# Kernel optimization log

Measured on AMD Instinct MI355X. Metric: run time of the kernel, lower is better.

Reference implementation:

```python
import jax, jax.numpy as jnp
import numpy as np

B, M, T, L, K = 64, 16, 2048, 64, 32
N = T - L + 1  # 1985 sliding-window positions


def setup_inputs() -> dict:
    key = jax.random.key(0)
    k1, k2, k3 = jax.random.split(key, 3)
    x = jax.random.normal(k1, (B, M, T), dtype=jnp.float32)
    # shapelets initialized uniform(-1, 1) as in nn.init.uniform_
    shapelets = jax.random.uniform(k2, (K, L), dtype=jnp.float32, minval=-1.0, maxval=1.0)
    # penalty maps (learned; zeros at init, random here for a non-trivial weighting)
    penalty_maps = 0.1 * jax.random.normal(k3, (K, M, N), dtype=jnp.float32)
    return {"x": x, "shapelets": shapelets, "penalty_maps": penalty_maps}


def reference(x, shapelets, penalty_maps):
    # x: (B, M, T); shapelets: (K, L); penalty_maps: (K, M, N)
    Lw = shapelets.shape[1]
    n_pos = x.shape[2] - Lw + 1
    # sliding-window view: (B, M, N, L), equivalent to torch unfold(dim=2, size=L, step=1)
    idx = jnp.arange(n_pos)[:, None] + jnp.arange(Lw)[None, :]
    sub = x[:, :, idx]  # (B, M, N, L)

    def per_shapelet(args):
        shp, pmap = args  # (L,), (M, N)
        # raw squared L2 distance over window, per channel/position: (B, M, N)
        raw = jnp.sum((sub - shp[None, None, None, :]) ** 2, axis=3)
        pen = jax.nn.elu(-pmap) + 2.0  # (M, N)
        wd = jnp.sum(raw * pen[None], axis=1)  # sum over channels -> (B, N)
        return jnp.min(wd, axis=1)  # min over positions -> (B,)

    # sequential map over the K shapelets avoids a Kx blow-up of the (B,M,N,L) intermediate
    feats = jax.lax.map(per_shapelet, (shapelets, penalty_maps))  # (K, B)
    return feats.T  # (B, K)
```

## Files before the change

### kernel.cpp

```cpp
#include <hip/hip_runtime.h>
#include <hip/hip_bf16.h>

#define B_ 64
#define M_ 16
#define T_ 2048
#define L_ 64
#define K_ 32
#define N_ (T_ - L_ + 1)
#define KMN (K_ * M_ * N_)
#define TN 64
#define NTH 256
#define XROW 144
#define STSTR 72
#define SQSTR 64

typedef __attribute__((ext_vector_type(8))) short bf16x8;
typedef __attribute__((ext_vector_type(4))) float f32x4;

__device__ __forceinline__ unsigned short f2bf(float f) {
    __hip_bfloat16 h = __float2bfloat16(f);
    return __builtin_bit_cast(unsigned short, h);
}

__global__ void pen_init_kernel(const float* __restrict__ pmap,
                                const float* __restrict__ shp,
                                float* __restrict__ pen,
                                float* __restrict__ ss_ws,
                                unsigned* __restrict__ out) {
    const int gid = blockIdx.x * 256 + threadIdx.x;
    if (gid < B_ * K_) out[gid] = 0x7F800000u;
    if (gid < K_) {
        float s = 0.f;
        for (int l = 0; l < L_; ++l) { float v = shp[gid * L_ + l]; s = fmaf(v, v, s); }
        ss_ws[gid] = s;
    }
    if (gid < KMN / 4) {
        const int i4 = gid * 4;
        float4 p = *(const float4*)(pmap + i4);
        float4 r;
        r.x = (p.x < 0.f) ? (2.f - p.x) : (__expf(-p.x) + 1.f);
        r.y = (p.y < 0.f) ? (2.f - p.y) : (__expf(-p.y) + 1.f);
        r.z = (p.z < 0.f) ? (2.f - p.z) : (__expf(-p.z) + 1.f);
        r.w = (p.w < 0.f) ? (2.f - p.w) : (__expf(-p.w) + 1.f);
        *(float4*)(pen + i4) = r;
    }
}

__global__ __launch_bounds__(NTH, 2)
void shapelet_mfma_kernel(const float* __restrict__ x,
                          const float* __restrict__ shp,
                          const float* __restrict__ pen,
                          const float* __restrict__ ss_ws,
                          unsigned* __restrict__ out) {
    __shared__ __align__(16) unsigned short xbuf4[M_][4][XROW];
    __shared__ __align__(16) unsigned short st[K_][STSTR];
    __shared__ __align__(16) float sqw[M_][SQSTR];

    const int tid = threadIdx.x;
    const int n0 = blockIdx.x * TN;
    const int b  = blockIdx.y;
    const bool fast = (n0 + 128 <= T_);

    const float* xb = x + ((size_t)b * M_) * T_ + n0;
    for (int g = tid; g < M_ * 31; g += NTH) {
        const int m = g / 31, j4 = (g - m * 31) * 4;
        const float* src = xb + m * T_ + j4;
        float h[8];
        if (fast) {
            float4 v0 = *(const float4*)src;
            float4 v1 = *(const float4*)(src + 4);
            h[0] = v0.x; h[1] = v0.y; h[2] = v0.z; h[3] = v0.w;
            h[4] = v1.x; h[5] = v1.y; h[6] = v1.z; h[7] = v1.w;
        } else {
#pragma unroll
            for (int i = 0; i < 8; ++i)
                h[i] = (n0 + j4 + i < T_) ? src[i] : 0.f;
        }
        unsigned short hb[8];
#pragma unroll
        for (int i = 0; i < 8; ++i) hb[i] = f2bf(h[i]);
#pragma unroll
        for (int s = 0; s < 4; ++s) {
            ushort4 sv = { hb[s], hb[s + 1], hb[s + 2], hb[s + 3] };
            *(ushort4*)&xbuf4[m][s][j4] = sv;
        }
    }
    for (int i = tid; i < K_ * 16; i += NTH) {
        const int k = i >> 4, l4 = (i & 15) * 4;
        float4 v = *(const float4*)(shp + k * L_ + l4);
        ushort4 sv = { f2bf(v.x), f2bf(v.y), f2bf(v.z), f2bf(v.w) };
        *(ushort4*)&st[k][l4] = sv;
    }
    if (tid < M_ * 8) {
        const int m = tid >> 3, j0 = (tid & 7) * 8;
        const float* xr = x + ((size_t)b * M_ + m) * T_ + n0;
        float s = 0.f;
        if (fast) {
#pragma unroll
            for (int qd = 0; qd < 16; ++qd) {
                float4 v = *(const float4*)(xr + j0 + qd * 4);
                s = fmaf(v.x, v.x, s); s = fmaf(v.y, v.y, s);
                s = fmaf(v.z, v.z, s); s = fmaf(v.w, v.w, s);
            }
            sqw[m][j0] = s;
#pragma unroll
            for (int d = 1; d < 8; ++d) {
                float a = xr[j0 + d + L_ - 1], r = xr[j0 + d - 1];
                s += a * a - r * r;
                sqw[m][j0 + d] = s;
            }
        } else {
            for (int l = 0; l < L_; ++l) {
                float v = (n0 + j0 + l < T_) ? xr[j0 + l] : 0.f;
                s = fmaf(v, v, s);
            }
            sqw[m][j0] = s;
            for (int d = 1; d < 8; ++d) {
                float a = (n0 + j0 + d + L_ - 1 < T_) ? xr[j0 + d + L_ - 1] : 0.f;
                float r = (n0 + j0 + d - 1 < T_) ? xr[j0 + d - 1] : 0.f;
                s += a * a - r * r;
                sqw[m][j0 + d] = s;
            }
        }
    }
    __syncthreads();

    const int lane = tid & 63;
    const int w  = tid >> 6;
    const int rl = lane & 15;
    const int q  = lane >> 4;
    const int sp = rl & 3;
    const int e0 = 16 * w + 8 * q + (rl & ~3);
    const int eq = e0 >> 2;
    const int nrow = n0 + 16 * w + 4 * q;

    bf16x8 bfr[2][2];
#pragma unroll
    for (int t = 0; t < 2; ++t)
#pragma unroll
        for (int h = 0; h < 2; ++h)
            bfr[t][h] = *(const bf16x8*)&st[16 * t + rl][8 * q + 32 * h];

    const float ssk0 = ss_ws[rl], ssk1 = ss_ws[16 + rl];

    const float* pr0 = pen + (size_t)rl * (M_ * N_) + nrow;
    const float* pr1 = pr0 + (size_t)16 * M_ * N_;

    f32x4 wd0 = (f32x4)0.f, wd1 = (f32x4)0.f;
    const f32x4 zero = (f32x4)0.f;

#pragma unroll 2
    for (int m = 0; m < M_; ++m) {
        float4 p0, p1;
        if (fast) {
            p0 = *(const float4*)(pr0 + (size_t)m * N_);
            p1 = *(const float4*)(pr1 + (size_t)m * N_);
        } else {
            p0 = make_float4(2.f, 2.f, 2.f, 2.f);
            p1 = make_float4(2.f, 2.f, 2.f, 2.f);
            const float* r0_ = pr0 + (size_t)m * N_;
            const float* r1_ = pr1 + (size_t)m * N_;
            if (nrow     < N_) { p0.x = r0_[0]; p1.x = r1_[0]; }
            if (nrow + 1 < N_) { p0.y = r0_[1]; p1.y = r1_[1]; }
            if (nrow + 2 < N_) { p0.z = r0_[2]; p1.z = r1_[2]; }
            if (nrow + 3 < N_) { p0.w = r0_[3]; p1.w = r1_[3]; }
        }

        const uint2* prow = (const uint2*)&xbuf4[m][sp][0];
        uint2 lo0 = prow[eq],     hi0 = prow[eq + 1];
        uint2 lo1 = prow[eq + 8], hi1 = prow[eq + 9];
        union { uint2 u2[2]; bf16x8 v; } fa0, fa1;
        fa0.u2[0] = lo0; fa0.u2[1] = hi0;
        fa1.u2[0] = lo1; fa1.u2[1] = hi1;

        f32x4 c0_ = __builtin_amdgcn_mfma_f32_16x16x32_bf16(fa0.v, bfr[0][0], zero, 0, 0, 0);
        c0_       = __builtin_amdgcn_mfma_f32_16x16x32_bf16(fa1.v, bfr[0][1], c0_, 0, 0, 0);
        f32x4 c1_ = __builtin_amdgcn_mfma_f32_16x16x32_bf16(fa0.v, bfr[1][0], zero, 0, 0, 0);
        c1_       = __builtin_amdgcn_mfma_f32_16x16x32_bf16(fa1.v, bfr[1][1], c1_, 0, 0, 0);

        f32x4 sq = *(const f32x4*)&sqw[m][16 * w + 4 * q];
        const float pe0[4] = { p0.x, p0.y, p0.z, p0.w };
        const float pe1[4] = { p1.x, p1.y, p1.z, p1.w };
#pragma unroll
        for (int r = 0; r < 4; ++r) {
            float t0v = fmaf(-2.f, c0_[r], sq[r] + ssk0);
            wd0[r] = fmaf(pe0[r], t0v, wd0[r]);
            float t1v = fmaf(-2.f, c1_[r], sq[r] + ssk1);
            wd1[r] = fmaf(pe1[r], t1v, wd1[r]);
        }
    }

#pragma unroll
    for (int t = 0; t < 2; ++t) {
        float lmin = __int_as_float(0x7F800000);
        const f32x4& wdv = t ? wd1 : wd0;
#pragma unroll
        for (int r = 0; r < 4; ++r) {
            if (nrow + r < N_) lmin = fminf(lmin, wdv[r]);
        }
        lmin = fminf(lmin, __shfl_xor(lmin, 16));
        lmin = fminf(lmin, __shfl_xor(lmin, 32));
        if (q == 0) {
            atomicMin(out + (size_t)b * K_ + 16 * t + rl,
                      __float_as_uint(fmaxf(lmin, 0.f)));
        }
    }
}

extern "C" void kernel_launch(void* const* d_in, const int* in_sizes, int n_in,
                              void* d_out, int out_size, void* d_ws, size_t ws_size,
                              hipStream_t stream) {
    const float* x    = (const float*)d_in[0];
    const float* shp  = (const float*)d_in[1];
    const float* pmap = (const float*)d_in[2];
    unsigned* out = (unsigned*)d_out;
    float* pen   = (float*)d_ws;
    float* ss_ws = pen + KMN;

    pen_init_kernel<<<dim3((KMN / 4 + 255) / 256), dim3(256), 0, stream>>>(
        pmap, shp, pen, ss_ws, out);

    dim3 grid((N_ + TN - 1) / TN, B_);
    shapelet_mfma_kernel<<<grid, dim3(NTH), 0, stream>>>(x, shp, pen, ss_ws, out);
}
```

Baseline: 100.8 us.

## Fuse penalty transform into main kernel and process four batches per block

Each block now handles four batch items, so every penalty-map value loaded and transformed through ELU is reused across four batches instead of being re-read once per batch. The separate pen_init kernel is gone: the ELU transform is computed inline, the shapelet norms are computed in shared memory, and output initialisation becomes a memset. The shapelet-norm term is hoisted out of the channel loop as ssk times the summed penalty. Channels are staged in two halves to keep shared memory small, and a block-level min reduction replaces per-wave atomics. The trade-offs are a 4x smaller grid (512 blocks, which may underfill the GPU), extra barriers between the two channel halves, and redundant exp work across blocks.

Measured after the change: 110.4 us. +9.5%, slower.

```diff
diff --git a/kernel.cpp b/kernel.cpp
--- a/kernel.cpp
+++ b/kernel.cpp
@@ -7,12 +7,12 @@
 #define L_ 64
 #define K_ 32
 #define N_ (T_ - L_ + 1)
-#define KMN (K_ * M_ * N_)
 #define TN 64
 #define NTH 256
+#define NB 4
+#define MSPLIT 8
 #define XROW 144
 #define STSTR 72
-#define SQSTR 64
 
 typedef __attribute__((ext_vector_type(8))) short bf16x8;
 typedef __attribute__((ext_vector_type(4))) float f32x4;
@@ -22,78 +22,64 @@
     return __builtin_bit_cast(unsigned short, h);
 }
 
-__global__ void pen_init_kernel(const float* __restrict__ pmap,
-                                const float* __restrict__ shp,
-                                float* __restrict__ pen,
-                                float* __restrict__ ss_ws,
-                                unsigned* __restrict__ out) {
-    const int gid = blockIdx.x * 256 + threadIdx.x;
-    if (gid < B_ * K_) out[gid] = 0x7F800000u;
-    if (gid < K_) {
-        float s = 0.f;
-        for (int l = 0; l < L_; ++l) { float v = shp[gid * L_ + l]; s = fmaf(v, v, s); }
-        ss_ws[gid] = s;
-    }
-    if (gid < KMN / 4) {
-        const int i4 = gid * 4;
-        float4 p = *(const float4*)(pmap + i4);
-        float4 r;
-        r.x = (p.x < 0.f) ? (2.f - p.x) : (__expf(-p.x) + 1.f);
-        r.y = (p.y < 0.f) ? (2.f - p.y) : (__expf(-p.y) + 1.f);
-        r.z = (p.z < 0.f) ? (2.f - p.z) : (__expf(-p.z) + 1.f);
-        r.w = (p.w < 0.f) ? (2.f - p.w) : (__expf(-p.w) + 1.f);
-        *(float4*)(pen + i4) = r;
-    }
-}
-
 __global__ __launch_bounds__(NTH, 2)
 void shapelet_mfma_kernel(const float* __restrict__ x,
                           const float* __restrict__ shp,
-                          const float* __restrict__ pen,
-                          const float* __restrict__ ss_ws,
+                          const float* __restrict__ pmap,
                           unsigned* __restrict__ out) {
-    __shared__ __align__(16) unsigned short xbuf4[M_][4][XROW];
+    __shared__ __align__(16) unsigned short xbuf4[NB][MSPLIT][4][XROW];
     __shared__ __align__(16) unsigned short st[K_][STSTR];
-    __shared__ __align__(16) float sqw[M_][SQSTR];
+    __shared__ __align__(16) float sqw[NB][MSPLIT][TN];
+    __shared__ float ssb[K_];
 
     const int tid = threadIdx.x;
     const int n0 = blockIdx.x * TN;
-    const int b  = blockIdx.y;
-    const bool fast = (n0 + 128 <= T_);
-
-    const float* xb = x + ((size_t)b * M_) * T_ + n0;
-    for (int g = tid; g < M_ * 31; g += NTH) {
-        const int m = g / 31, j4 = (g - m * 31) * 4;
-        const float* src = xb + m * T_ + j4;
-        float h[8];
-        if (fast) {
-            float4 v0 = *(const float4*)src;
-            float4 v1 = *(const float4*)(src + 4);
-            h[0] = v0.x; h[1] = v0.y; h[2] = v0.z; h[3] = v0.w;
-            h[4] = v1.x; h[5] = v1.y; h[6] = v1.z; h[7] = v1.w;
-        } else {
-#pragma unroll
-            for (int i = 0; i < 8; ++i)
-                h[i] = (n0 + j4 + i < T_) ? src[i] : 0.f;
-        }
-        unsigned short hb[8];
-#pragma unroll
-        for (int i = 0; i < 8; ++i) hb[i] = f2bf(h[i]);
-#pragma unroll
-        for (int s = 0; s < 4; ++s) {
-            ushort4 sv = { hb[s], hb[s + 1], hb[s + 2], hb[s + 3] };
-            *(ushort4*)&xbuf4[m][s][j4] = sv;
-        }
-    }
+    const int b0 = blockIdx.y * NB;
+    const bool fast = (n0 + 2 * TN <= T_);
+
     for (int i = tid; i < K_ * 16; i += NTH) {
         const int k = i >> 4, l4 = (i & 15) * 4;
         float4 v = *(const float4*)(shp + k * L_ + l4);
         ushort4 sv = { f2bf(v.x), f2bf(v.y), f2bf(v.z), f2bf(v.w) };
         *(ushort4*)&st[k][l4] = sv;
     }
-    if (tid < M_ * 8) {
-        const int m = tid >> 3, j0 = (tid & 7) * 8;
-        const float* xr = x + ((size_t)b * M_ + m) * T_ + n0;
+    if (tid < K_) {
+        float s = 0.f;
+        for (int l = 0; l < L_; ++l) { float v = shp[tid * L_ + l]; s = fmaf(v, v, s); }
+        ssb[tid] = s;
+    }
+
+    auto stage = [&](int p) {
+        for (int g = tid; g < NB * MSPLIT * 31; g += NTH) {
+            const int bb = g / (MSPLIT * 31);
+            const int rem = g - bb * (MSPLIT * 31);
+            const int mm = rem / 31;
+            const int j4 = (rem - mm * 31) * 4;
+            const int m = p * MSPLIT + mm;
+            const float* src = x + ((size_t)(b0 + bb) * M_ + m) * T_ + n0 + j4;
+            float h[8];
+            if (fast) {
+                float4 v0 = *(const float4*)src;
+                float4 v1 = *(const float4*)(src + 4);
+                h[0] = v0.x; h[1] = v0.y; h[2] = v0.z; h[3] = v0.w;
+                h[4] = v1.x; h[5] = v1.y; h[6] = v1.z; h[7] = v1.w;
+            } else {
+#pragma unroll
+                for (int i = 0; i < 8; ++i)
+                    h[i] = (n0 + j4 + i < T_) ? src[i] : 0.f;
+            }
+            unsigned short hb[8];
+#pragma unroll
+            for (int i = 0; i < 8; ++i) hb[i] = f2bf(h[i]);
+#pragma unroll
+            for (int s = 0; s < 4; ++s) {
+                ushort4 sv = { hb[s], hb[s + 1], hb[s + 2], hb[s + 3] };
+                *(ushort4*)&xbuf4[bb][mm][s][j4] = sv;
+            }
+        }
+        const int bb = tid >> 6, mm = (tid >> 3) & 7, j0 = (tid & 7) * 8;
+        const int m = p * MSPLIT + mm;
+        const float* xr = x + ((size_t)(b0 + bb) * M_ + m) * T_ + n0;
         float s = 0.f;
         if (fast) {
 #pragma unroll
@@ -102,27 +88,29 @@
                 s = fmaf(v.x, v.x, s); s = fmaf(v.y, v.y, s);
                 s = fmaf(v.z, v.z, s); s = fmaf(v.w, v.w, s);
             }
-            sqw[m][j0] = s;
+            sqw[bb][mm][j0] = s;
 #pragma unroll
             for (int d = 1; d < 8; ++d) {
                 float a = xr[j0 + d + L_ - 1], r = xr[j0 + d - 1];
                 s += a * a - r * r;
-                sqw[m][j0 + d] = s;
+                sqw[bb][mm][j0 + d] = s;
             }
         } else {
             for (int l = 0; l < L_; ++l) {
                 float v = (n0 + j0 + l < T_) ? xr[j0 + l] : 0.f;
                 s = fmaf(v, v, s);
             }
-            sqw[m][j0] = s;
+            sqw[bb][mm][j0] = s;
             for (int d = 1; d < 8; ++d) {
                 float a = (n0 + j0 + d + L_ - 1 < T_) ? xr[j0 + d + L_ - 1] : 0.f;
                 float r = (n0 + j0 + d - 1 < T_) ? xr[j0 + d - 1] : 0.f;
                 s += a * a - r * r;
-                sqw[m][j0 + d] = s;
-            }
-        }
-    }
+                sqw[bb][mm][j0 + d] = s;
+            }
+        }
+    };
+
+    stage(0);
     __syncthreads();
 
     const int lane = tid & 63;
@@ -141,69 +129,108 @@
         for (int h = 0; h < 2; ++h)
             bfr[t][h] = *(const bf16x8*)&st[16 * t + rl][8 * q + 32 * h];
 
-    const float ssk0 = ss_ws[rl], ssk1 = ss_ws[16 + rl];
-
-    const float* pr0 = pen + (size_t)rl * (M_ * N_) + nrow;
+    const float ssk0 = ssb[rl], ssk1 = ssb[16 + rl];
+
+    const float* pr0 = pmap + (size_t)rl * (M_ * N_) + nrow;
     const float* pr1 = pr0 + (size_t)16 * M_ * N_;
 
-    f32x4 wd0 = (f32x4)0.f, wd1 = (f32x4)0.f;
+    f32x4 wd0[NB], wd1[NB];
+#pragma unroll
+    for (int bb = 0; bb < NB; ++bb) { wd0[bb] = (f32x4)0.f; wd1[bb] = (f32x4)0.f; }
+    f32x4 P0 = (f32x4)0.f, P1 = (f32x4)0.f;
     const f32x4 zero = (f32x4)0.f;
 
+    for (int p = 0; p < 2; ++p) {
+        if (p) {
+            __syncthreads();
+            stage(1);
+            __syncthreads();
+        }
 #pragma unroll 2
-    for (int m = 0; m < M_; ++m) {
-        float4 p0, p1;
-        if (fast) {
-            p0 = *(const float4*)(pr0 + (size_t)m * N_);
-            p1 = *(const float4*)(pr1 + (size_t)m * N_);
-        } else {
-            p0 = make_float4(2.f, 2.f, 2.f, 2.f);
-            p1 = make_float4(2.f, 2.f, 2.f, 2.f);
-            const float* r0_ = pr0 + (size_t)m * N_;
-            const float* r1_ = pr1 + (size_t)m * N_;
-            if (nrow     < N_) { p0.x = r0_[0]; p1.x = r1_[0]; }
-            if (nrow + 1 < N_) { p0.y = r0_[1]; p1.y = r1_[1]; }
-            if (nrow + 2 < N_) { p0.z = r0_[2]; p1.z = r1_[2]; }
-            if (nrow + 3 < N_) { p0.w = r0_[3]; p1.w = r1_[3]; }
-        }
-
-        const uint2* prow = (const uint2*)&xbuf4[m][sp][0];
-        uint2 lo0 = prow[eq],     hi0 = prow[eq + 1];
-        uint2 lo1 = prow[eq + 8], hi1 = prow[eq + 9];
-        union { uint2 u2[2]; bf16x8 v; } fa0, fa1;
-        fa0.u2[0] = lo0; fa0.u2[1] = hi0;
-        fa1.u2[0] = lo1; fa1.u2[1] = hi1;
-
-        f32x4 c0_ = __builtin_amdgcn_mfma_f32_16x16x32_bf16(fa0.v, bfr[0][0], zero, 0, 0, 0);
-        c0_       = __builtin_amdgcn_mfma_f32_16x16x32_bf16(fa1.v, bfr[0][1], c0_, 0, 0, 0);
-        f32x4 c1_ = __builtin_amdgcn_mfma_f32_16x16x32_bf16(fa0.v, bfr[1][0], zero, 0, 0, 0);
-        c1_       = __builtin_amdgcn_mfma_f32_16x16x32_bf16(fa1.v, bfr[1][1], c1_, 0, 0, 0);
-
-        f32x4 sq = *(const f32x4*)&sqw[m][16 * w + 4 * q];
-        const float pe0[4] = { p0.x, p0.y, p0.z, p0.w };
-        const float pe1[4] = { p1.x, p1.y, p1.z, p1.w };
+        for (int mm = 0; mm < MSPLIT; ++mm) {
+            const int m = p * MSPLIT + mm;
+            float4 pm0, pm1;
+            if (fast) {
+                pm0 = *(const float4*)(pr0 + (size_t)m * N_);
+                pm1 = *(const float4*)(pr1 + (size_t)m * N_);
+            } else {
+                pm0 = make_float4(0.f, 0.f, 0.f, 0.f);
+                pm1 = make_float4(0.f, 0.f, 0.f, 0.f);
+                const float* r0_ = pr0 + (size_t)m * N_;
+                const float* r1_ = pr1 + (size_t)m * N_;
+                if (nrow     < N_) { pm0.x = r0_[0]; pm1.x = r1_[0]; }
+                if (nrow + 1 < N_) { pm0.y = r0_[1]; pm1.y = r1_[1]; }
+                if (nrow + 2 < N_) { pm0.z = r0_[2]; pm1.z = r1_[2]; }
+                if (nrow + 3 < N_) { pm0.w = r0_[3]; pm1.w = r1_[3]; }
+            }
+            float pe0[4], pe1[4];
+            {
+                const float pv0[4] = { pm0.x, pm0.y, pm0.z, pm0.w };
+                const float pv1[4] = { pm1.x, pm1.y, pm1.z, pm1.w };
+#pragma unroll
+                for (int r = 0; r < 4; ++r) {
+                    pe0[r] = (pv0[r] < 0.f) ? (2.f - pv0[r]) : (__expf(-pv0[r]) + 1.f);
+                    pe1[r] = (pv1[r] < 0.f) ? (2.f - pv1[r]) : (__expf(-pv1[r]) + 1.f);
+                    P0[r] += pe0[r];
+                    P1[r] += pe1[r];
+                }
+            }
+#pragma unroll
+            for (int bb = 0; bb < NB; ++bb) {
+                const uint2* prow = (const uint2*)&xbuf4[bb][mm][sp][0];
+                uint2 lo0 = prow[eq],     hi0 = prow[eq + 1];
+                uint2 lo1 = prow[eq + 8], hi1 = prow[eq + 9];
+                union { uint2 u2[2]; bf16x8 v; } fa0, fa1;
+                fa0.u2[0] = lo0; fa0.u2[1] = hi0;
+                fa1.u2[0] = lo1; fa1.u2[1] = hi1;
+
+                f32x4 c0_ = __builtin_amdgcn_mfma_f32_16x16x32_bf16(fa0.v, bfr[0][0], zero, 0, 0, 0);
+                c0_       = __builtin_amdgcn_mfma_f32_16x16x32_bf16(fa1.v, bfr[0][1], c0_, 0, 0, 0);
+                f32x4 c1_ = __builtin_amdgcn_mfma_f32_16x16x32_bf16(fa0.v, bfr[1][0], zero, 0, 0, 0);
+                c1_       = __builtin_amdgcn_mfma_f32_16x16x32_bf16(fa1.v, bfr[1][1], c1_, 0, 0, 0);
+
+                f32x4 sq = *(const f32x4*)&sqw[bb][mm][16 * w + 4 * q];
+#pragma unroll
+                for (int r = 0; r < 4; ++r) {
+                    float u0 = fmaf(-2.f, c0_[r], sq[r]);
+                    wd0[bb][r] = fmaf(pe0[r], u0, wd0[bb][r]);
+                    float u1 = fmaf(-2.f, c1_[r], sq[r]);
+                    wd1[bb][r] = fmaf(pe1[r], u1, wd1[bb][r]);
+                }
+            }
+        }
+    }
+
+#pragma unroll
+    for (int bb = 0; bb < NB; ++bb)
 #pragma unroll
         for (int r = 0; r < 4; ++r) {
-            float t0v = fmaf(-2.f, c0_[r], sq[r] + ssk0);
-            wd0[r] = fmaf(pe0[r], t0v, wd0[r]);
-            float t1v = fmaf(-2.f, c1_[r], sq[r] + ssk1);
-            wd1[r] = fmaf(pe1[r], t1v, wd1[r]);
-        }
-    }
-
-#pragma unroll
-    for (int t = 0; t < 2; ++t) {
-        float lmin = __int_as_float(0x7F800000);
-        const f32x4& wdv = t ? wd1 : wd0;
-#pragma unroll
-        for (int r = 0; r < 4; ++r) {
-            if (nrow + r < N_) lmin = fminf(lmin, wdv[r]);
-        }
-        lmin = fminf(lmin, __shfl_xor(lmin, 16));
-        lmin = fminf(lmin, __shfl_xor(lmin, 32));
-        if (q == 0) {
-            atomicMin(out + (size_t)b * K_ + 16 * t + rl,
-                      __float_as_uint(fmaxf(lmin, 0.f)));
-        }
+            wd0[bb][r] = fmaf(ssk0, P0[r], wd0[bb][r]);
+            wd1[bb][r] = fmaf(ssk1, P1[r], wd1[bb][r]);
+        }
+
+    __syncthreads();
+    float* red = (float*)&sqw[0][0][0];
+#pragma unroll
+    for (int bb = 0; bb < NB; ++bb) {
+#pragma unroll
+        for (int t = 0; t < 2; ++t) {
+            float lmin = __int_as_float(0x7F800000);
+            const f32x4 wdv = t ? wd1[bb] : wd0[bb];
+#pragma unroll
+            for (int r = 0; r < 4; ++r)
+                if (nrow + r < N_) lmin = fminf(lmin, wdv[r]);
+            lmin = fminf(lmin, __shfl_xor(lmin, 16));
+            lmin = fminf(lmin, __shfl_xor(lmin, 32));
+            if (q == 0) red[w * 128 + bb * 32 + t * 16 + rl] = lmin;
+        }
+    }
+    __syncthreads();
+    if (tid < 128) {
+        float v = fminf(fminf(red[tid], red[128 + tid]),
+                        fminf(red[256 + tid], red[384 + tid]));
+        const int bb = tid >> 5, kk = tid & 31;
+        atomicMin(out + (size_t)(b0 + bb) * K_ + kk, __float_as_uint(fmaxf(v, 0.f)));
     }
 }
 
@@ -214,12 +241,10 @@
     const float* shp  = (const float*)d_in[1];
     const float* pmap = (const float*)d_in[2];
     unsigned* out = (unsigned*)d_out;
-    float* pen   = (float*)d_ws;
-    float* ss_ws = pen + KMN;
-
-    pen_init_kernel<<<dim3((KMN / 4 + 255) / 256), dim3(256), 0, stream>>>(
-        pmap, shp, pen, ss_ws, out);
-
-    dim3 grid((N_ + TN - 1) / TN, B_);
-    shapelet_mfma_kernel<<<grid, dim3(NTH), 0, stream>>>(x, shp, pen, ss_ws, out);
+    (void)d_ws; (void)ws_size;
+
+    hipMemsetAsync(d_out, 0xFF, (size_t)B_ * K_ * sizeof(unsigned), stream);
+
+    dim3 grid((N_ + TN - 1) / TN, B_ / NB);
+    shapelet_mfma_kernel<<<grid, dim3(NTH), 0, stream>>>(x, shp, pmap, out);
 }
```

## Fuse ELU penalty and shapelet norms into main kernel, drop init pass

Applied to the files above, without the earlier changes.

Removes the separate pre-pass kernel that wrote a full transformed penalty map to workspace. The main kernel now reads the raw penalty map and applies the ELU transform inline, and each block computes the shapelet squared norms itself. The output is initialised with a memset instead. It also adds a block-level min reduction through shared memory, so only one atomic per shapelet is issued per block, fully unrolls the fast loop and raises the launch-bounds occupancy hint. The cost is that the exp for the penalty is recomputed for every batch element, and register pressure may rise under the tighter occupancy hint.

Result: slower. 247.3 us (+145.3%).

```diff
diff --git a/kernel.cpp b/kernel.cpp
--- a/kernel.cpp
+++ b/kernel.cpp
@@ -7,12 +7,10 @@
 #define L_ 64
 #define K_ 32
 #define N_ (T_ - L_ + 1)
-#define KMN (K_ * M_ * N_)
 #define TN 64
 #define NTH 256
 #define XROW 144
 #define STSTR 72
-#define SQSTR 64
 
 typedef __attribute__((ext_vector_type(8))) short bf16x8;
 typedef __attribute__((ext_vector_type(4))) float f32x4;
@@ -22,44 +20,36 @@
     return __builtin_bit_cast(unsigned short, h);
 }
 
-__global__ void pen_init_kernel(const float* __restrict__ pmap,
-                                const float* __restrict__ shp,
-                                float* __restrict__ pen,
-                                float* __restrict__ ss_ws,
-                                unsigned* __restrict__ out) {
-    const int gid = blockIdx.x * 256 + threadIdx.x;
-    if (gid < B_ * K_) out[gid] = 0x7F800000u;
-    if (gid < K_) {
-        float s = 0.f;
-        for (int l = 0; l < L_; ++l) { float v = shp[gid * L_ + l]; s = fmaf(v, v, s); }
-        ss_ws[gid] = s;
-    }
-    if (gid < KMN / 4) {
-        const int i4 = gid * 4;
-        float4 p = *(const float4*)(pmap + i4);
-        float4 r;
-        r.x = (p.x < 0.f) ? (2.f - p.x) : (__expf(-p.x) + 1.f);
-        r.y = (p.y < 0.f) ? (2.f - p.y) : (__expf(-p.y) + 1.f);
-        r.z = (p.z < 0.f) ? (2.f - p.z) : (__expf(-p.z) + 1.f);
-        r.w = (p.w < 0.f) ? (2.f - p.w) : (__expf(-p.w) + 1.f);
-        *(float4*)(pen + i4) = r;
-    }
-}
-
-__global__ __launch_bounds__(NTH, 2)
+__device__ __forceinline__ float elu_pen(float p) {
+    return (p < 0.f) ? (2.f - p) : (__expf(-p) + 1.f);
+}
+
+__global__ __launch_bounds__(NTH, 6)
 void shapelet_mfma_kernel(const float* __restrict__ x,
                           const float* __restrict__ shp,
-                          const float* __restrict__ pen,
-                          const float* __restrict__ ss_ws,
+                          const float* __restrict__ pmap,
                           unsigned* __restrict__ out) {
     __shared__ __align__(16) unsigned short xbuf4[M_][4][XROW];
     __shared__ __align__(16) unsigned short st[K_][STSTR];
-    __shared__ __align__(16) float sqw[M_][SQSTR];
+    __shared__ __align__(16) float sqw[M_][TN];
+    __shared__ float ssb[K_];
 
     const int tid = threadIdx.x;
     const int n0 = blockIdx.x * TN;
     const int b  = blockIdx.y;
-    const bool fast = (n0 + 128 <= T_);
+    const bool fast = (n0 + 2 * TN <= T_);
+
+    for (int i = tid; i < K_ * 16; i += NTH) {
+        const int k = i >> 4, l4 = (i & 15) * 4;
+        float4 v = *(const float4*)(shp + k * L_ + l4);
+        ushort4 sv = { f2bf(v.x), f2bf(v.y), f2bf(v.z), f2bf(v.w) };
+        *(ushort4*)&st[k][l4] = sv;
+    }
+    if (tid < K_) {
+        float s = 0.f;
+        for (int l = 0; l < L_; ++l) { float v = shp[tid * L_ + l]; s = fmaf(v, v, s); }
+        ssb[tid] = s;
+    }
 
     const float* xb = x + ((size_t)b * M_) * T_ + n0;
     for (int g = tid; g < M_ * 31; g += NTH) {
@@ -85,12 +75,6 @@
             *(ushort4*)&xbuf4[m][s][j4] = sv;
         }
     }
-    for (int i = tid; i < K_ * 16; i += NTH) {
-        const int k = i >> 4, l4 = (i & 15) * 4;
-        float4 v = *(const float4*)(shp + k * L_ + l4);
-        ushort4 sv = { f2bf(v.x), f2bf(v.y), f2bf(v.z), f2bf(v.w) };
-        *(ushort4*)&st[k][l4] = sv;
-    }
     if (tid < M_ * 8) {
         const int m = tid >> 3, j0 = (tid & 7) * 8;
         const float* xr = x + ((size_t)b * M_ + m) * T_ + n0;
@@ -141,69 +125,102 @@
         for (int h = 0; h < 2; ++h)
             bfr[t][h] = *(const bf16x8*)&st[16 * t + rl][8 * q + 32 * h];
 
-    const float ssk0 = ss_ws[rl], ssk1 = ss_ws[16 + rl];
-
-    const float* pr0 = pen + (size_t)rl * (M_ * N_) + nrow;
+    const float ssk0 = ssb[rl], ssk1 = ssb[16 + rl];
+
+    const float* pr0 = pmap + (size_t)rl * (M_ * N_) + nrow;
     const float* pr1 = pr0 + (size_t)16 * M_ * N_;
 
     f32x4 wd0 = (f32x4)0.f, wd1 = (f32x4)0.f;
     const f32x4 zero = (f32x4)0.f;
 
+    if (fast) {
+#pragma unroll
+        for (int m = 0; m < M_; ++m) {
+            float4 pm0 = *(const float4*)(pr0 + (size_t)m * N_);
+            float4 pm1 = *(const float4*)(pr1 + (size_t)m * N_);
+
+            const uint2* prow = (const uint2*)&xbuf4[m][sp][0];
+            uint2 lo0 = prow[eq],     hi0 = prow[eq + 1];
+            uint2 lo1 = prow[eq + 8], hi1 = prow[eq + 9];
+            union { uint2 u2[2]; bf16x8 v; } fa0, fa1;
+            fa0.u2[0] = lo0; fa0.u2[1] = hi0;
+            fa1.u2[0] = lo1; fa1.u2[1] = hi1;
+
+            f32x4 c0_ = __builtin_amdgcn_mfma_f32_16x16x32_bf16(fa0.v, bfr[0][0], zero, 0, 0, 0);
+            c0_       = __builtin_amdgcn_mfma_f32_16x16x32_bf16(fa1.v, bfr[0][1], c0_, 0, 0, 0);
+            f32x4 c1_ = __builtin_amdgcn_mfma_f32_16x16x32_bf16(fa0.v, bfr[1][0], zero, 0, 0, 0);
+            c1_       = __builtin_amdgcn_mfma_f32_16x16x32_bf16(fa1.v, bfr[1][1], c1_, 0, 0, 0);
+
+            const float pv0[4] = { pm0.x, pm0.y, pm0.z, pm0.w };
+            const float pv1[4] = { pm1.x, pm1.y, pm1.z, pm1.w };
+            f32x4 sq = *(const f32x4*)&sqw[m][16 * w + 4 * q];
+#pragma unroll
+            for (int r = 0; r < 4; ++r) {
+                float pe0 = elu_pen(pv0[r]);
+                float pe1 = elu_pen(pv1[r]);
+                float u0 = fmaf(-2.f, c0_[r], sq[r] + ssk0);
+                wd0[r] = fmaf(pe0, u0, wd0[r]);
+                float u1 = fmaf(-2.f, c1_[r], sq[r] + ssk1);
+                wd1[r] = fmaf(pe1, u1, wd1[r]);
+            }
+        }
+    } else {
 #pragma unroll 2
-    for (int m = 0; m < M_; ++m) {
-        float4 p0, p1;
-        if (fast) {
-            p0 = *(const float4*)(pr0 + (size_t)m * N_);
-            p1 = *(const float4*)(pr1 + (size_t)m * N_);
-        } else {
-            p0 = make_float4(2.f, 2.f, 2.f, 2.f);
-            p1 = make_float4(2.f, 2.f, 2.f, 2.f);
+        for (int m = 0; m < M_; ++m) {
+            float4 pm0 = make_float4(0.f, 0.f, 0.f, 0.f);
+            float4 pm1 = make_float4(0.f, 0.f, 0.f, 0.f);
             const float* r0_ = pr0 + (size_t)m * N_;
             const float* r1_ = pr1 + (size_t)m * N_;
-            if (nrow     < N_) { p0.x = r0_[0]; p1.x = r1_[0]; }
-            if (nrow + 1 < N_) { p0.y = r0_[1]; p1.y = r1_[1]; }
-            if (nrow + 2 < N_) { p0.z = r0_[2]; p1.z = r1_[2]; }
-            if (nrow + 3 < N_) { p0.w = r0_[3]; p1.w = r1_[3]; }
-        }
-
-        const uint2* prow = (const uint2*)&xbuf4[m][sp][0];
-        uint2 lo0 = prow[eq],     hi0 = prow[eq + 1];
-        uint2 lo1 = prow[eq + 8], hi1 = prow[eq + 9];
-        union { uint2 u2[2]; bf16x8 v; } fa0, fa1;
-        fa0.u2[0] = lo0; fa0.u2[1] = hi0;
-        fa1.u2[0] = lo1; fa1.u2[1] = hi1;
-
-        f32x4 c0_ = __builtin_amdgcn_mfma_f32_16x16x32_bf16(fa0.v, bfr[0][0], zero, 0, 0, 0);
-        c0_       = __builtin_amdgcn_mfma_f32_16x16x32_bf16(fa1.v, bfr[0][1], c0_, 0, 0, 0);
-        f32x4 c1_ = __builtin_amdgcn_mfma_f32_16x16x32_bf16(fa0.v, bfr[1][0], zero, 0, 0, 0);
-        c1_       = __builtin_amdgcn_mfma_f32_16x16x32_bf16(fa1.v, bfr[1][1], c1_, 0, 0, 0);
-
-        f32x4 sq = *(const f32x4*)&sqw[m][16 * w + 4 * q];
-        const float pe0[4] = { p0.x, p0.y, p0.z, p0.w };
-        const float pe1[4] = { p1.x, p1.y, p1.z, p1.w };
-#pragma unroll
-        for (int r = 0; r < 4; ++r) {
-            float t0v = fmaf(-2.f, c0_[r], sq[r] + ssk0);
-            wd0[r] = fmaf(pe0[r], t0v, wd0[r]);
-            float t1v = fmaf(-2.f, c1_[r], sq[r] + ssk1);
-            wd1[r] = fmaf(pe1[r], t1v, wd1[r]);
-        }
-    }
-
+            if (nrow     < N_) { pm0.x = r0_[0]; pm1.x = r1_[0]; }
+            if (nrow + 1 < N_) { pm0.y = r0_[1]; pm1.y = r1_[1]; }
+            if (nrow + 2 < N_) { pm0.z = r0_[2]; pm1.z = r1_[2]; }
+            if (nrow + 3 < N_) { pm0.w = r0_[3]; pm1.w = r1_[3]; }
+
+            const uint2* prow = (const uint2*)&xbuf4[m][sp][0];
+            uint2 lo0 = prow[eq],     hi0 = prow[eq + 1];
+            uint2 lo1 = prow[eq + 8], hi1 = prow[eq + 9];
+            union { uint2 u2[2]; bf16x8 v; } fa0, fa1;
+            fa0.u2[0] = lo0; fa0.u2[1] = hi0;
+            fa1.u2[0] = lo1; fa1.u2[1] = hi1;
+
+            f32x4 c0_ = __builtin_amdgcn_mfma_f32_16x16x32_bf16(fa0.v, bfr[0][0], zero, 0, 0, 0);
+            c0_       = __builtin_amdgcn_mfma_f32_16x16x32_bf16(fa1.v, bfr[0][1], c0_, 0, 0, 0);
+            f32x4 c1_ = __builtin_amdgcn_mfma_f32_16x16x32_bf16(fa0.v, bfr[1][0], zero, 0, 0, 0);
+            c1_       = __builtin_amdgcn_mfma_f32_16x16x32_bf16(fa1.v, bfr[1][1], c1_, 0, 0, 0);
+
+            const float pv0[4] = { pm0.x, pm0.y, pm0.z, pm0.w };
+            const float pv1[4] = { pm1.x, pm1.y, pm1.z, pm1.w };
+            f32x4 sq = *(const f32x4*)&sqw[m][16 * w + 4 * q];
+#pragma unroll
+            for (int r = 0; r < 4; ++r) {
+                float pe0 = elu_pen(pv0[r]);
+                float pe1 = elu_pen(pv1[r]);
+                float u0 = fmaf(-2.f, c0_[r], sq[r] + ssk0);
+                wd0[r] = fmaf(pe0, u0, wd0[r]);
+                float u1 = fmaf(-2.f, c1_[r], sq[r] + ssk1);
+                wd1[r] = fmaf(pe1, u1, wd1[r]);
+            }
+        }
+    }
+
+    __syncthreads();
+    float* red = (float*)&sqw[0][0];
 #pragma unroll
     for (int t = 0; t < 2; ++t) {
         float lmin = __int_as_float(0x7F800000);
-        const f32x4& wdv = t ? wd1 : wd0;
-#pragma unroll
-        for (int r = 0; r < 4; ++r) {
+        const f32x4 wdv = t ? wd1 : wd0;
+#pragma unroll
+        for (int r = 0; r < 4; ++r)
             if (nrow + r < N_) lmin = fminf(lmin, wdv[r]);
-        }
         lmin = fminf(lmin, __shfl_xor(lmin, 16));
         lmin = fminf(lmin, __shfl_xor(lmin, 32));
-        if (q == 0) {
-            atomicMin(out + (size_t)b * K_ + 16 * t + rl,
-                      __float_as_uint(fmaxf(lmin, 0.f)));
-        }
+        if (q == 0) red[w * 32 + t * 16 + rl] = lmin;
+    }
+    __syncthreads();
+    if (tid < K_) {
+        float v = fminf(fminf(red[tid], red[32 + tid]),
+                        fminf(red[64 + tid], red[96 + tid]));
+        atomicMin(out + (size_t)b * K_ + tid, __float_as_uint(fmaxf(v, 0.f)));
     }
 }
 
@@ -214,12 +231,10 @@
     const float* shp  = (const float*)d_in[1];
     const float* pmap = (const float*)d_in[2];
     unsigned* out = (unsigned*)d_out;
-    float* pen   = (float*)d_ws;
-    float* ss_ws = pen + KMN;
-
-    pen_init_kernel<<<dim3((KMN / 4 + 255) / 256), dim3(256), 0, stream>>>(
-        pmap, shp, pen, ss_ws, out);
+    (void)d_ws; (void)ws_size;
+
+    hipMemsetAsync(d_out, 0xFF, (size_t)B_ * K_ * sizeof(unsigned), stream);
 
     dim3 grid((N_ + TN - 1) / TN, B_);
-    shapelet_mfma_kernel<<<grid, dim3(NTH), 0, stream>>>(x, shp, pen, ss_ws, out);
-}
+    shapelet_mfma_kernel<<<grid, dim3(NTH), 0, stream>>>(x, shp, pmap, out);
+}
```

## Process four batches per block to amortize shapelet setup and cut atomics

Applied to the files above, without the earlier changes.

Each block now loops over four batch indices in turn, so the bf16 shapelet tile, its fragments and the shapelet norms are loaded once and reused across batches. The per-batch minimum is reduced across the four waves in shared memory before a single atomicMin per shapelet, replacing per-wave atomics. The penalty precompute kernel handles two float4 items per thread with half the grid. In exchange the grid shrinks fourfold, to about 496 blocks, and each batch iteration adds extra barriers. Penalty loads still go to global memory or cache for every batch.

New measurement: 109.6 us. 8.8% more time.

```diff
diff --git a/kernel.cpp b/kernel.cpp
--- a/kernel.cpp
+++ b/kernel.cpp
@@ -10,6 +10,7 @@
 #define KMN (K_ * M_ * N_)
 #define TN 64
 #define NTH 256
+#define NBSEQ 4
 #define XROW 144
 #define STSTR 72
 #define SQSTR 64
@@ -34,15 +35,19 @@
         for (int l = 0; l < L_; ++l) { float v = shp[gid * L_ + l]; s = fmaf(v, v, s); }
         ss_ws[gid] = s;
     }
-    if (gid < KMN / 4) {
-        const int i4 = gid * 4;
-        float4 p = *(const float4*)(pmap + i4);
-        float4 r;
-        r.x = (p.x < 0.f) ? (2.f - p.x) : (__expf(-p.x) + 1.f);
-        r.y = (p.y < 0.f) ? (2.f - p.y) : (__expf(-p.y) + 1.f);
-        r.z = (p.z < 0.f) ? (2.f - p.z) : (__expf(-p.z) + 1.f);
-        r.w = (p.w < 0.f) ? (2.f - p.w) : (__expf(-p.w) + 1.f);
-        *(float4*)(pen + i4) = r;
+#pragma unroll
+    for (int half = 0; half < 2; ++half) {
+        const int item = gid + half * (KMN / 8);
+        if (item < KMN / 4) {
+            const int i4 = item * 4;
+            float4 p = *(const float4*)(pmap + i4);
+            float4 r;
+            r.x = (p.x < 0.f) ? (2.f - p.x) : (__expf(-p.x) + 1.f);
+            r.y = (p.y < 0.f) ? (2.f - p.y) : (__expf(-p.y) + 1.f);
+            r.z = (p.z < 0.f) ? (2.f - p.z) : (__expf(-p.z) + 1.f);
+            r.w = (p.w < 0.f) ? (2.f - p.w) : (__expf(-p.w) + 1.f);
+            *(float4*)(pen + i4) = r;
+        }
     }
 }
 
@@ -57,73 +62,9 @@
     __shared__ __align__(16) float sqw[M_][SQSTR];
 
     const int tid = threadIdx.x;
-    const int n0 = blockIdx.x * TN;
-    const int b  = blockIdx.y;
+    const int bx = blockIdx.x;
+    const int n0 = bx * TN;
     const bool fast = (n0 + 128 <= T_);
-
-    const float* xb = x + ((size_t)b * M_) * T_ + n0;
-    for (int g = tid; g < M_ * 31; g += NTH) {
-        const int m = g / 31, j4 = (g - m * 31) * 4;
-        const float* src = xb + m * T_ + j4;
-        float h[8];
-        if (fast) {
-            float4 v0 = *(const float4*)src;
-            float4 v1 = *(const float4*)(src + 4);
-            h[0] = v0.x; h[1] = v0.y; h[2] = v0.z; h[3] = v0.w;
-            h[4] = v1.x; h[5] = v1.y; h[6] = v1.z; h[7] = v1.w;
-        } else {
-#pragma unroll
-            for (int i = 0; i < 8; ++i)
-                h[i] = (n0 + j4 + i < T_) ? src[i] : 0.f;
-        }
-        unsigned short hb[8];
-#pragma unroll
-        for (int i = 0; i < 8; ++i) hb[i] = f2bf(h[i]);
-#pragma unroll
-        for (int s = 0; s < 4; ++s) {
-            ushort4 sv = { hb[s], hb[s + 1], hb[s + 2], hb[s + 3] };
-            *(ushort4*)&xbuf4[m][s][j4] = sv;
-        }
-    }
-    for (int i = tid; i < K_ * 16; i += NTH) {
-        const int k = i >> 4, l4 = (i & 15) * 4;
-        float4 v = *(const float4*)(shp + k * L_ + l4);
-        ushort4 sv = { f2bf(v.x), f2bf(v.y), f2bf(v.z), f2bf(v.w) };
-        *(ushort4*)&st[k][l4] = sv;
-    }
-    if (tid < M_ * 8) {
-        const int m = tid >> 3, j0 = (tid & 7) * 8;
-        const float* xr = x + ((size_t)b * M_ + m) * T_ + n0;
-        float s = 0.f;
-        if (fast) {
-#pragma unroll
-            for (int qd = 0; qd < 16; ++qd) {
-                float4 v = *(const float4*)(xr + j0 + qd * 4);
-                s = fmaf(v.x, v.x, s); s = fmaf(v.y, v.y, s);
-                s = fmaf(v.z, v.z, s); s = fmaf(v.w, v.w, s);
-            }
-            sqw[m][j0] = s;
-#pragma unroll
-            for (int d = 1; d < 8; ++d) {
-                float a = xr[j0 + d + L_ - 1], r = xr[j0 + d - 1];
-                s += a * a - r * r;
-                sqw[m][j0 + d] = s;
-            }
-        } else {
-            for (int l = 0; l < L_; ++l) {
-                float v = (n0 + j0 + l < T_) ? xr[j0 + l] : 0.f;
-                s = fmaf(v, v, s);
-            }
-            sqw[m][j0] = s;
-            for (int d = 1; d < 8; ++d) {
-                float a = (n0 + j0 + d + L_ - 1 < T_) ? xr[j0 + d + L_ - 1] : 0.f;
-                float r = (n0 + j0 + d - 1 < T_) ? xr[j0 + d - 1] : 0.f;
-                s += a * a - r * r;
-                sqw[m][j0 + d] = s;
-            }
-        }
-    }
-    __syncthreads();
 
     const int lane = tid & 63;
     const int w  = tid >> 6;
@@ -134,6 +75,15 @@
     const int eq = e0 >> 2;
     const int nrow = n0 + 16 * w + 4 * q;
 
+    for (int i = tid; i < K_ * 16; i += NTH) {
+        const int k = i >> 4, l4 = (i & 15) * 4;
+        float4 v = *(const float4*)(shp + k * L_ + l4);
+        ushort4 sv = { f2bf(v.x), f2bf(v.y), f2bf(v.z), f2bf(v.w) };
+        *(ushort4*)&st[k][l4] = sv;
+    }
+    const float ssk0 = ss_ws[rl], ssk1 = ss_ws[16 + rl];
+    __syncthreads();
+
     bf16x8 bfr[2][2];
 #pragma unroll
     for (int t = 0; t < 2; ++t)
@@ -141,69 +91,136 @@
         for (int h = 0; h < 2; ++h)
             bfr[t][h] = *(const bf16x8*)&st[16 * t + rl][8 * q + 32 * h];
 
-    const float ssk0 = ss_ws[rl], ssk1 = ss_ws[16 + rl];
-
-    const float* pr0 = pen + (size_t)rl * (M_ * N_) + nrow;
-    const float* pr1 = pr0 + (size_t)16 * M_ * N_;
-
-    f32x4 wd0 = (f32x4)0.f, wd1 = (f32x4)0.f;
+    const float* pr0_base = pen + (size_t)rl * (M_ * N_) + nrow;
     const f32x4 zero = (f32x4)0.f;
 
+    for (int bb = 0; bb < NBSEQ; ++bb) {
+        const int b = blockIdx.y * NBSEQ + bb;
+
+        const float* xb = x + ((size_t)b * M_) * T_ + n0;
+        for (int g = tid; g < M_ * 31; g += NTH) {
+            const int m = g / 31, j4 = (g - m * 31) * 4;
+            const float* src = xb + m * T_ + j4;
+            float h[8];
+            if (fast) {
+                float4 v0 = *(const float4*)src;
+                float4 v1 = *(const float4*)(src + 4);
+                h[0] = v0.x; h[1] = v0.y; h[2] = v0.z; h[3] = v0.w;
+                h[4] = v1.x; h[5] = v1.y; h[6] = v1.z; h[7] = v1.w;
+            } else {
+#pragma unroll
+                for (int i = 0; i < 8; ++i)
+                    h[i] = (n0 + j4 + i < T_) ? src[i] : 0.f;
+            }
+            unsigned short hb[8];
+#pragma unroll
+            for (int i = 0; i < 8; ++i) hb[i] = f2bf(h[i]);
+#pragma unroll
+            for (int s = 0; s < 4; ++s) {
+                ushort4 sv = { hb[s], hb[s + 1], hb[s + 2], hb[s + 3] };
+                *(ushort4*)&xbuf4[m][s][j4] = sv;
+            }
+        }
+        if (tid < M_ * 8) {
+            const int m = tid >> 3, j0 = (tid & 7) * 8;
+            const float* xr = x + ((size_t)b * M_ + m) * T_ + n0;
+            float s = 0.f;
+            if (fast) {
+#pragma unroll
+                for (int qd = 0; qd < 16; ++qd) {
+                    float4 v = *(const float4*)(xr + j0 + qd * 4);
+                    s = fmaf(v.x, v.x, s); s = fmaf(v.y, v.y, s);
+                    s = fmaf(v.z, v.z, s); s = fmaf(v.w, v.w, s);
+                }
+                sqw[m][j0] = s;
+#pragma unroll
+                for (int d = 1; d < 8; ++d) {
+                    float a = xr[j0 + d + L_ - 1], r = xr[j0 + d - 1];
+                    s += a * a - r * r;
+                    sqw[m][j0 + d] = s;
+                }
+            } else {
+                for (int l = 0; l < L_; ++l) {
+                    float v = (n0 + j0 + l < T_) ? xr[j0 + l] : 0.f;
+                    s = fmaf(v, v, s);
+                }
+                sqw[m][j0] = s;
+                for (int d = 1; d < 8; ++d) {
+                    float a = (n0 + j0 + d + L_ - 1 < T_) ? xr[j0 + d + L_ - 1] : 0.f;
+                    float r = (n0 + j0 + d - 1 < T_) ? xr[j0 + d - 1] : 0.f;
+                    s += a * a - r * r;
+                    sqw[m][j0 + d] = s;
+                }
+            }
+        }
+        __syncthreads();
+
+        const float* pr0 = pr0_base;
+        const float* pr1 = pr0 + (size_t)16 * M_ * N_;
+
+        f32x4 wd0 = (f32x4)0.f, wd1 = (f32x4)0.f;
+
 #pragma unroll 2
-    for (int m = 0; m < M_; ++m) {
-        float4 p0, p1;
-        if (fast) {
-            p0 = *(const float4*)(pr0 + (size_t)m * N_);
-            p1 = *(const float4*)(pr1 + (size_t)m * N_);
-        } else {
-            p0 = make_float4(2.f, 2.f, 2.f, 2.f);
-            p1 = make_float4(2.f, 2.f, 2.f, 2.f);
-            const float* r0_ = pr0 + (size_t)m * N_;
-            const float* r1_ = pr1 + (size_t)m * N_;
-            if (nrow     < N_) { p0.x = r0_[0]; p1.x = r1_[0]; }
-            if (nrow + 1 < N_) { p0.y = r0_[1]; p1.y = r1_[1]; }
-            if (nrow + 2 < N_) { p0.z = r0_[2]; p1.z = r1_[2]; }
-            if (nrow + 3 < N_) { p0.w = r0_[3]; p1.w = r1_[3]; }
-        }
-
-        const uint2* prow = (const uint2*)&xbuf4[m][sp][0];
-        uint2 lo0 = prow[eq],     hi0 = prow[eq + 1];
-        uint2 lo1 = prow[eq + 8], hi1 = prow[eq + 9];
-        union { uint2 u2[2]; bf16x8 v; } fa0, fa1;
-        fa0.u2[0] = lo0; fa0.u2[1] = hi0;
-        fa1.u2[0] = lo1; fa1.u2[1] = hi1;
-
-        f32x4 c0_ = __builtin_amdgcn_mfma_f32_16x16x32_bf16(fa0.v, bfr[0][0], zero, 0, 0, 0);
-        c0_       = __builtin_amdgcn_mfma_f32_16x16x32_bf16(fa1.v, bfr[0][1], c0_, 0, 0, 0);
-        f32x4 c1_ = __builtin_amdgcn_mfma_f32_16x16x32_bf16(fa0.v, bfr[1][0], zero, 0, 0, 0);
-        c1_       = __builtin_amdgcn_mfma_f32_16x16x32_bf16(fa1.v, bfr[1][1], c1_, 0, 0, 0);
-
-        f32x4 sq = *(const f32x4*)&sqw[m][16 * w + 4 * q];
-        const float pe0[4] = { p0.x, p0.y, p0.z, p0.w };
-        const float pe1[4] = { p1.x, p1.y, p1.z, p1.w };
-#pragma unroll
-        for (int r = 0; r < 4; ++r) {
-            float t0v = fmaf(-2.f, c0_[r], sq[r] + ssk0);
-            wd0[r] = fmaf(pe0[r], t0v, wd0[r]);
-            float t1v = fmaf(-2.f, c1_[r], sq[r] + ssk1);
-            wd1[r] = fmaf(pe1[r], t1v, wd1[r]);
-        }
-    }
-
-#pragma unroll
-    for (int t = 0; t < 2; ++t) {
-        float lmin = __int_as_float(0x7F800000);
-        const f32x4& wdv = t ? wd1 : wd0;
-#pragma unroll
-        for (int r = 0; r < 4; ++r) {
-            if (nrow + r < N_) lmin = fminf(lmin, wdv[r]);
-        }
-        lmin = fminf(lmin, __shfl_xor(lmin, 16));
-        lmin = fminf(lmin, __shfl_xor(lmin, 32));
-        if (q == 0) {
-            atomicMin(out + (size_t)b * K_ + 16 * t + rl,
-                      __float_as_uint(fmaxf(lmin, 0.f)));
-        }
+        for (int m = 0; m < M_; ++m) {
+            float4 p0, p1;
+            if (fast) {
+                p0 = *(const float4*)(pr0 + (size_t)m * N_);
+                p1 = *(const float4*)(pr1 + (size_t)m * N_);
+            } else {
+                p0 = make_float4(2.f, 2.f, 2.f, 2.f);
+                p1 = make_float4(2.f, 2.f, 2.f, 2.f);
+                const float* r0_ = pr0 + (size_t)m * N_;
+                const float* r1_ = pr1 + (size_t)m * N_;
+                if (nrow     < N_) { p0.x = r0_[0]; p1.x = r1_[0]; }
+                if (nrow + 1 < N_) { p0.y = r0_[1]; p1.y = r1_[1]; }
+                if (nrow + 2 < N_) { p0.z = r0_[2]; p1.z = r1_[2]; }
+                if (nrow + 3 < N_) { p0.w = r0_[3]; p1.w = r1_[3]; }
+            }
+
+            const uint2* prow = (const uint2*)&xbuf4[m][sp][0];
+            uint2 lo0 = prow[eq],     hi0 = prow[eq + 1];
+            uint2 lo1 = prow[eq + 8], hi1 = prow[eq + 9];
+            union { uint2 u2[2]; bf16x8 v; } fa0, fa1;
+            fa0.u2[0] = lo0; fa0.u2[1] = hi0;
+            fa1.u2[0] = lo1; fa1.u2[1] = hi1;
+
+            f32x4 c0_ = __builtin_amdgcn_mfma_f32_16x16x32_bf16(fa0.v, bfr[0][0], zero, 0, 0, 0);
+            c0_       = __builtin_amdgcn_mfma_f32_16x16x32_bf16(fa1.v, bfr[0][1], c0_, 0, 0, 0);
+            f32x4 c1_ = __builtin_amdgcn_mfma_f32_16x16x32_bf16(fa0.v, bfr[1][0], zero, 0, 0, 0);
+            c1_       = __builtin_amdgcn_mfma_f32_16x16x32_bf16(fa1.v, bfr[1][1], c1_, 0, 0, 0);
+
+            f32x4 sq = *(const f32x4*)&sqw[m][16 * w + 4 * q];
+            const float pe0[4] = { p0.x, p0.y, p0.z, p0.w };
+            const float pe1[4] = { p1.x, p1.y, p1.z, p1.w };
+#pragma unroll
+            for (int r = 0; r < 4; ++r) {
+                float t0v = fmaf(-2.f, c0_[r], sq[r] + ssk0);
+                wd0[r] = fmaf(pe0[r], t0v, wd0[r]);
+                float t1v = fmaf(-2.f, c1_[r], sq[r] + ssk1);
+                wd1[r] = fmaf(pe1[r], t1v, wd1[r]);
+            }
+        }
+
+        __syncthreads();
+        float* red = (float*)&sqw[0][0];
+#pragma unroll
+        for (int t = 0; t < 2; ++t) {
+            float lmin = __int_as_float(0x7F800000);
+            const f32x4 wdv = t ? wd1 : wd0;
+#pragma unroll
+            for (int r = 0; r < 4; ++r)
+                if (nrow + r < N_) lmin = fminf(lmin, wdv[r]);
+            lmin = fminf(lmin, __shfl_xor(lmin, 16));
+            lmin = fminf(lmin, __shfl_xor(lmin, 32));
+            if (q == 0) red[w * 32 + t * 16 + rl] = lmin;
+        }
+        __syncthreads();
+        if (tid < K_) {
+            float v = fminf(fminf(red[tid], red[32 + tid]),
+                            fminf(red[64 + tid], red[96 + tid]));
+            atomicMin(out + (size_t)b * K_ + tid, __float_as_uint(fmaxf(v, 0.f)));
+        }
+        __syncthreads();
     }
 }
 
@@ -217,9 +234,9 @@
     float* pen   = (float*)d_ws;
     float* ss_ws = pen + KMN;
 
-    pen_init_kernel<<<dim3((KMN / 4 + 255) / 256), dim3(256), 0, stream>>>(
+    pen_init_kernel<<<dim3((KMN / 8 + 255) / 256), dim3(256), 0, stream>>>(
         pmap, shp, pen, ss_ws, out);
 
-    dim3 grid((N_ + TN - 1) / TN, B_);
+    dim3 grid((N_ + TN - 1) / TN, B_ / NBSEQ);
     shapelet_mfma_kernel<<<grid, dim3(NTH), 0, stream>>>(x, shp, pen, ss_ws, out);
 }
```
